# Optimization experiments

Hardware: AMD Instinct MI355X
Metric: run time of the kernel (lower is better)

## Reference

```python
import jax, jax.numpy as jnp
import numpy as np

B, CIN, COUT, H, W = 4, 256, 128, 64, 64

def conv1x1(x, w, b):
    # x: [B,C,H,W], w: [O,C], b: [O]
    return jnp.einsum('bchw,oc->bohw', x, w) + b[None, :, None, None]

def setup_inputs() -> dict:
    key = jax.random.key(0)
    ks = jax.random.split(key, 9)
    s_in = 1.0 / np.sqrt(CIN)
    s_out = 1.0 / np.sqrt(COUT)
    return {
        'x': jax.random.normal(ks[0], (B, CIN, H, W), dtype=jnp.float32),
        'w_theta': jax.random.normal(ks[1], (COUT, CIN), dtype=jnp.float32) * s_in,
        'b_theta': jax.random.normal(ks[2], (COUT,), dtype=jnp.float32) * s_in,
        'w_phi': jax.random.normal(ks[3], (COUT, CIN), dtype=jnp.float32) * s_in,
        'b_phi': jax.random.normal(ks[4], (COUT,), dtype=jnp.float32) * s_in,
        'w_g': jax.random.normal(ks[5], (COUT, CIN), dtype=jnp.float32) * s_in,
        'b_g': jax.random.normal(ks[6], (COUT,), dtype=jnp.float32) * s_in,
        'w_W': jax.random.normal(ks[7], (CIN, COUT), dtype=jnp.float32) * s_out,
        'b_W': jax.random.normal(ks[8], (CIN,), dtype=jnp.float32) * s_out,
    }

def reference(x, w_theta, b_theta, w_phi, b_phi, w_g, b_g, w_W, b_W):
    b, c, h, w = x.shape
    n = h * w
    co = w_theta.shape[0]
    theta_x = conv1x1(x, w_theta, b_theta).reshape(b, co, n).transpose(0, 2, 1)  # [B,N,Co]
    phi_x = conv1x1(x, w_phi, b_phi).reshape(b, co, n)                            # [B,Co,N]
    g_x = conv1x1(x, w_g, b_g).reshape(b, co, n).transpose(0, 2, 1)               # [B,N,Co]
    scores = jnp.einsum('bnc,bcm->bnm', theta_x, phi_x)                           # [B,N,N]
    attn = jax.nn.softmax(scores, axis=-1)
    y = jnp.einsum('bnm,bmc->bnc', attn, g_x)                                     # [B,N,Co]
    y = y.transpose(0, 2, 1).reshape(b, co, h, w)
    z = conv1x1(y, w_W, b_W) + x
    return z
```

## Files before the change

### kernel.cpp

```cpp
#include <hip/hip_runtime.h>

#define B_    4
#define C_    256
#define O_    128
#define N_    4096
#define THW   256
#define TILES 64

typedef __attribute__((ext_vector_type(8))) _Float16 f16x8;
typedef __attribute__((ext_vector_type(4))) float    f32x4;

struct __align__(8) us4 { unsigned short x, y, z, w; };

__device__ __forceinline__ float bf2f(unsigned short u) {
    unsigned v = ((unsigned)u) << 16;
    union { unsigned u; float f; } c; c.u = v; return c.f;
}
__device__ __forceinline__ unsigned short f2bf(float f) {
    union { float f; unsigned u; } c; c.f = f;
    unsigned r = c.u + 0x7fffu + ((c.u >> 16) & 1u);
    return (unsigned short)(r >> 16);
}
__device__ __forceinline__ unsigned short f2h(float f) {
    _Float16 h = (_Float16)f;
    union { _Float16 h; unsigned short s; } c; c.h = h; return c.s;
}
__device__ __forceinline__ float h2f(unsigned short s) {
    union { unsigned short s; _Float16 h; } c; c.s = s; return (float)c.h;
}

__device__ __forceinline__ void load4f(const void* base, size_t idx, int isf32, float o[4]) {
    if (isf32) {
        float4 v = *(const float4*)((const float*)base + idx);
        o[0] = v.x; o[1] = v.y; o[2] = v.z; o[3] = v.w;
    } else {
        us4 v = *(const us4*)((const unsigned short*)base + idx);
        o[0] = bf2f(v.x); o[1] = bf2f(v.y); o[2] = bf2f(v.z); o[3] = bf2f(v.w);
    }
}
__device__ __forceinline__ float load1f(const void* base, size_t idx, int isf32) {
    return isf32 ? ((const float*)base)[idx] : bf2f(((const unsigned short*)base)[idx]);
}

__global__ __launch_bounds__(256) void detect_kernel(
    const unsigned short* __restrict__ xu, int* __restrict__ flag)
{
    __shared__ int cnt;
    if (threadIdx.x == 0) cnt = 0;
    __syncthreads();
    int local = 0;
    for (int i = threadIdx.x; i < 4096; i += 256) {
        unsigned short u = xu[2 * i];
        int e = (u >> 7) & 0xFF;
        if (e == 0xFF || e >= 0x90 || (e > 0 && e <= 0x60)) local++;
    }
    atomicAdd(&cnt, local);
    __syncthreads();
    if (threadIdx.x == 0) *flag = (cnt > 1024) ? 1 : 0;
}

__global__ __launch_bounds__(256) void qkv_kernel(
    const void* __restrict__ x,
    const void* __restrict__ wt, const void* __restrict__ wp,
    const void* __restrict__ wg,
    const void* __restrict__ bt, const void* __restrict__ bp,
    const void* __restrict__ bg,
    const int*  __restrict__ flag,
    unsigned short* __restrict__ thph,
    unsigned short* __restrict__ gT)
{
    const int isf32 = *flag;
    const int jsel = blockIdx.y;
    const void* w  = jsel == 0 ? wt : (jsel == 1 ? wp : wg);
    const void* bi = jsel == 0 ? bt : (jsel == 1 ? bp : bg);
    const int b  = blockIdx.z;
    const int n0 = blockIdx.x * 64;
    const int tid  = threadIdx.x;
    const int wv   = tid >> 6, lane = tid & 63;
    const int quad = lane >> 4, l16 = lane & 15;

    __shared__ alignas(16) unsigned short smem[64 * 72 + 128 * 72];
    unsigned short (*As)[72] = (unsigned short(*)[72])smem;
    unsigned short (*Bs)[72] = (unsigned short(*)[72])(smem + 64 * 72);

    f32x4 acc[8];
    for (int i = 0; i < 8; i++) acc[i] = (f32x4)0.f;

    for (int kc = 0; kc < C_; kc += 64) {
        __syncthreads();
        for (int it = 0; it < 4; it++) {
            int l = it * 256 + tid;
            int c = l >> 4;
            int ng = l & 15;
            float v[4];
            load4f(x, (size_t)(b * C_ + kc + c) * N_ + n0 + ng * 4, isf32, v);
            int g = c >> 3, cl = c & 7;
            int swz = ((g ^ (ng & 7)) << 3) + cl;
            As[ng * 4 + 0][swz] = f2h(v[0]);
            As[ng * 4 + 1][swz] = f2h(v[1]);
            As[ng * 4 + 2][swz] = f2h(v[2]);
            As[ng * 4 + 3][swz] = f2h(v[3]);
        }
        for (int it = 0; it < 8; it++) {
            int l = it * 256 + tid;
            int j = l >> 4;
            int cg = l & 15;
            float v[4];
            load4f(w, (size_t)j * C_ + kc + cg * 4, isf32, v);
            Bs[j][cg * 4 + 0] = f2h(v[0]);
            Bs[j][cg * 4 + 1] = f2h(v[1]);
            Bs[j][cg * 4 + 2] = f2h(v[2]);
            Bs[j][cg * 4 + 3] = f2h(v[3]);
        }
        __syncthreads();
        for (int s = 0; s < 2; s++) {
            int row = wv * 16 + l16;
            int g2 = ((s * 4 + quad) ^ ((row >> 2) & 7)) << 3;
            f16x8 a = *(const f16x8*)&As[row][g2];
            for (int jt = 0; jt < 8; jt++) {
                f16x8 bb = *(const f16x8*)&Bs[jt * 16 + l16][s * 32 + quad * 8];
                acc[jt] = __builtin_amdgcn_mfma_f32_16x16x32_f16(a, bb, acc[jt], 0, 0, 0);
            }
        }
    }

    if (jsel < 2) {
        for (int jt = 0; jt < 8; jt++) {
            int j = jt * 16 + l16;
            float bias = load1f(bi, j, isf32);
            for (int r = 0; r < 4; r++) {
                int n = n0 + wv * 16 + quad * 4 + r;
                thph[(size_t)(b * N_ + n) * THW + jsel * O_ + j] = f2h(acc[jt][r] + bias);
            }
        }
    } else {
        unsigned short (*T)[68] = (unsigned short(*)[68])smem;
        __syncthreads();
        for (int jt = 0; jt < 8; jt++) {
            int j = jt * 16 + l16;
            float bias = load1f(bi, j, isf32);
            for (int r = 0; r < 4; r++) {
                int nl = wv * 16 + quad * 4 + r;
                T[j][nl] = f2h(acc[jt][r] + bias);
            }
        }
        __syncthreads();
        for (int it = 0; it < 8; it++) {
            int l = it * 256 + tid;
            int j = l >> 4;
            int ng = l & 15;
            *(us4*)(gT + ((size_t)(b * O_ + j)) * N_ + n0 + ng * 4) = *(const us4*)&T[j][ng * 4];
        }
    }
}

__global__ __launch_bounds__(512, 4) void attn_partial(
    const unsigned short* __restrict__ thph,
    const unsigned short* __restrict__ gT,
    unsigned short* __restrict__ partO,
    float* __restrict__ pm,
    float* __restrict__ pl,
    int S)
{
    const int b    = blockIdx.z;
    const int s_id = blockIdx.y;
    const int n0   = blockIdx.x * 128;
    const int tid  = threadIdx.x;
    const int wv   = tid >> 6, lane = tid & 63;
    const int quad = lane >> 4, l16 = lane & 15;

    const int t0 = (TILES * s_id) / S;
    const int t1 = (TILES * (s_id + 1)) / S;

    __shared__ alignas(16) unsigned short Ks[64][136];
    __shared__ alignas(16) unsigned short Gs[128][72];
    __shared__ alignas(16) unsigned short Ps[8][16][72];

    f16x8 qf[4];
    {
        int qrow = n0 + wv * 16 + l16;
        const unsigned short* qp = thph + (size_t)(b * N_ + qrow) * THW;
        for (int s = 0; s < 4; s++)
            qf[s] = *(const f16x8*)(qp + s * 32 + quad * 8);
    }

    f32x4 oacc[8];
    for (int i = 0; i < 8; i++) oacc[i] = (f32x4)0.f;
    float mstate = -INFINITY, lstate = 0.f;

    us4 kreg[4], greg[4];
    auto prefetch = [&](int mt) {
        int m0 = mt * 64;
        #pragma unroll
        for (int it = 0; it < 4; it++) {
            int l = it * 512 + tid;
            int mm = l >> 5, og = l & 31;
            kreg[it] = *(const us4*)(thph + (size_t)(b * N_ + m0 + mm) * THW + O_ + og * 4);
        }
        #pragma unroll
        for (int it = 0; it < 4; it++) {
            int l = it * 512 + tid;
            int o = l >> 4, ng = l & 15;
            greg[it] = *(const us4*)(gT + ((size_t)(b * O_ + o)) * N_ + m0 + ng * 4);
        }
    };
    prefetch(t0);

    for (int mt = t0; mt < t1; mt++) {
        __syncthreads();
        #pragma unroll
        for (int it = 0; it < 4; it++) {
            int l = it * 512 + tid;
            int mm = l >> 5, og = l & 31;
            *(us4*)&Ks[mm][og * 4] = kreg[it];
        }
        #pragma unroll
        for (int it = 0; it < 4; it++) {
            int l = it * 512 + tid;
            int o = l >> 4, ng = l & 15;
            *(us4*)&Gs[o][ng * 4] = greg[it];
        }
        __syncthreads();
        if (mt + 1 < t1) prefetch(mt + 1);

        f32x4 sacc[4];
        for (int kt = 0; kt < 4; kt++) sacc[kt] = (f32x4)0.f;
        for (int s = 0; s < 4; s++) {
            for (int kt = 0; kt < 4; kt++) {
                f16x8 kb = *(const f16x8*)&Ks[kt * 16 + l16][s * 32 + quad * 8];
                sacc[kt] = __builtin_amdgcn_mfma_f32_16x16x32_f16(kb, qf[s], sacc[kt], 0, 0, 0);
            }
        }

        float rm = fmaxf(fmaxf(fmaxf(sacc[0][0], sacc[0][1]), fmaxf(sacc[0][2], sacc[0][3])),
                         fmaxf(fmaxf(sacc[1][0], sacc[1][1]), fmaxf(sacc[1][2], sacc[1][3])));
        rm = fmaxf(rm, fmaxf(fmaxf(fmaxf(sacc[2][0], sacc[2][1]), fmaxf(sacc[2][2], sacc[2][3])),
                             fmaxf(fmaxf(sacc[3][0], sacc[3][1]), fmaxf(sacc[3][2], sacc[3][3]))));
        rm = fmaxf(rm, __shfl_xor(rm, 16));
        rm = fmaxf(rm, __shfl_xor(rm, 32));

        float mnew  = fmaxf(mstate, rm);
        float alpha = __expf(mstate - mnew);
        mstate = mnew;

        float rs = 0.f;
        #pragma unroll
        for (int kt = 0; kt < 4; kt++) {
            float p0 = __expf(sacc[kt][0] - mnew);
            float p1 = __expf(sacc[kt][1] - mnew);
            float p2 = __expf(sacc[kt][2] - mnew);
            float p3 = __expf(sacc[kt][3] - mnew);
            rs += (p0 + p1) + (p2 + p3);
            us4 pk;
            pk.x = f2h(p0); pk.y = f2h(p1); pk.z = f2h(p2); pk.w = f2h(p3);
            *(us4*)&Ps[wv][l16][kt * 16 + quad * 4] = pk;
        }
        rs += __shfl_xor(rs, 16);
        rs += __shfl_xor(rs, 32);
        lstate = lstate * alpha + rs;

        float av[4];
        #pragma unroll
        for (int r = 0; r < 4; r++) av[r] = __shfl(alpha, quad * 4 + r);
        #pragma unroll
        for (int jt = 0; jt < 8; jt++)
            #pragma unroll
            for (int r = 0; r < 4; r++) oacc[jt][r] *= av[r];

        for (int s = 0; s < 2; s++) {
            f16x8 pa = *(const f16x8*)&Ps[wv][l16][s * 32 + quad * 8];
            for (int jt = 0; jt < 8; jt++) {
                f16x8 gb = *(const f16x8*)&Gs[jt * 16 + l16][s * 32 + quad * 8];
                oacc[jt] = __builtin_amdgcn_mfma_f32_16x16x32_f16(pa, gb, oacc[jt], 0, 0, 0);
            }
        }
    }

    for (int r = 0; r < 4; r++) {
        int n = n0 + wv * 16 + quad * 4 + r;
        size_t rowb = ((size_t)(s_id * B_ + b) * N_ + n) * O_;
        for (int jt = 0; jt < 8; jt++)
            partO[rowb + jt * 16 + l16] = f2h(oacc[jt][r]);
    }
    if (quad == 0) {
        int n = n0 + wv * 16 + l16;
        pm[(size_t)(s_id * B_ + b) * N_ + n] = mstate;
        pl[(size_t)(s_id * B_ + b) * N_ + n] = lstate;
    }
}

__global__ __launch_bounds__(256) void merge_kernel(
    const unsigned short* __restrict__ partO,
    const float* __restrict__ pm, const float* __restrict__ pl,
    unsigned short* __restrict__ y,
    int S)
{
    int idx = blockIdx.x * 256 + threadIdx.x;
    int bn  = idx >> 5;
    int og  = idx & 31;
    const int BN = B_ * N_;

    float M = -INFINITY;
    for (int s = 0; s < S; s++) M = fmaxf(M, pm[(size_t)s * BN + bn]);
    float w[4];
    float L = 0.f;
    for (int s = 0; s < S; s++) {
        w[s] = __expf(pm[(size_t)s * BN + bn] - M);
        L += w[s] * pl[(size_t)s * BN + bn];
    }
    float inv = 1.0f / L;

    float a0 = 0.f, a1 = 0.f, a2 = 0.f, a3 = 0.f;
    for (int s = 0; s < S; s++) {
        us4 v = *(const us4*)(partO + ((size_t)s * BN + bn) * O_ + og * 4);
        a0 += h2f(v.x) * w[s];
        a1 += h2f(v.y) * w[s];
        a2 += h2f(v.z) * w[s];
        a3 += h2f(v.w) * w[s];
    }
    us4 r;
    r.x = f2h(a0 * inv); r.y = f2h(a1 * inv);
    r.z = f2h(a2 * inv); r.w = f2h(a3 * inv);
    *(us4*)(y + (size_t)bn * O_ + og * 4) = r;
}

__global__ __launch_bounds__(256) void out_kernel(
    const unsigned short* __restrict__ y,
    const void* __restrict__ wW,
    const void* __restrict__ bW,
    const void* __restrict__ x,
    const int*  __restrict__ flag,
    void* __restrict__ z)
{
    const int isf32 = *flag;
    const int b  = blockIdx.z;
    const int c0 = blockIdx.y * 64;
    const int n0 = blockIdx.x * 128;
    const int tid  = threadIdx.x;
    const int wv   = tid >> 6, lane = tid & 63;
    const int quad = lane >> 4, l16 = lane & 15;

    __shared__ alignas(16) unsigned short Ys[128][136];
    __shared__ alignas(16) unsigned short Ws[64][136];

    for (int it = 0; it < 16; it++) {
        int l = it * 256 + tid;
        int nn = l >> 5;
        int og = l & 31;
        us4 v = *(const us4*)(y + (size_t)(b * N_ + n0 + nn) * O_ + og * 4);
        *(us4*)&Ys[nn][og * 4] = v;
    }
    for (int it = 0; it < 8; it++) {
        int l = it * 256 + tid;
        int cc = l >> 5;
        int og = l & 31;
        float v[4];
        load4f(wW, (size_t)(c0 + cc) * O_ + og * 4, isf32, v);
        Ws[cc][og * 4 + 0] = f2h(v[0]);
        Ws[cc][og * 4 + 1] = f2h(v[1]);
        Ws[cc][og * 4 + 2] = f2h(v[2]);
        Ws[cc][og * 4 + 3] = f2h(v[3]);
    }
    __syncthreads();

    f32x4 acc[8];
    for (int i = 0; i < 8; i++) acc[i] = (f32x4)0.f;
    for (int s = 0; s < 4; s++) {
        f16x8 a = *(const f16x8*)&Ws[wv * 16 + l16][s * 32 + quad * 8];
        for (int nt = 0; nt < 8; nt++) {
            f16x8 bb = *(const f16x8*)&Ys[nt * 16 + l16][s * 32 + quad * 8];
            acc[nt] = __builtin_amdgcn_mfma_f32_16x16x32_f16(a, bb, acc[nt], 0, 0, 0);
        }
    }
    for (int r = 0; r < 4; r++) {
        int c = c0 + wv * 16 + quad * 4 + r;
        float bias = load1f(bW, c, isf32);
        for (int nt = 0; nt < 8; nt++) {
            int n = n0 + nt * 16 + l16;
            size_t idx = (size_t)(b * C_ + c) * N_ + n;
            float zv = acc[nt][r] + bias + load1f(x, idx, isf32);
            if (isf32) ((float*)z)[idx] = zv;
            else       ((unsigned short*)z)[idx] = f2bf(zv);
        }
    }
}

extern "C" void kernel_launch(void* const* d_in, const int* in_sizes, int n_in,
                              void* d_out, int out_size, void* d_ws, size_t ws_size,
                              hipStream_t stream) {
    const void* x  = d_in[0];
    const void* wt = d_in[1];
    const void* bt = d_in[2];
    const void* wp = d_in[3];
    const void* bp = d_in[4];
    const void* wg = d_in[5];
    const void* bg = d_in[6];
    const void* wW = d_in[7];
    const void* bW = d_in[8];

    const size_t base = 64 + 8388608  + 4194304 ;
    const size_t per_split = 4194304  + 131072 ;
    int S = 4;
    while (S > 1 && base + (size_t)S * per_split > ws_size) S--;

    char* p = (char*)d_ws;
    int* flag = (int*)p;                    p += 64;
    unsigned short* thph = (unsigned short*)p;  p += 8388608;
    unsigned short* gT   = (unsigned short*)p;  p += 4194304;
    unsigned short* partO = (unsigned short*)p; p += (size_t)S * 4194304;
    float* pm = (float*)p;                  p += (size_t)S * 65536;
    float* pl = (float*)p;
    unsigned short* y = gT;

    detect_kernel<<<1, 256, 0, stream>>>((const unsigned short*)x, flag);

    dim3 g1(N_ / 64, 3, B_);
    qkv_kernel<<<g1, 256, 0, stream>>>(x, wt, wp, wg, bt, bp, bg, flag, thph, gT);

    dim3 g2(N_ / 128, S, B_);
    attn_partial<<<g2, 512, 0, stream>>>(thph, gT, partO, pm, pl, S);

    merge_kernel<<<(B_ * N_ * 32) / 256, 256, 0, stream>>>(partO, pm, pl, y, S);

    dim3 g3(N_ / 128, C_ / 64, B_);
    out_kernel<<<g3, 256, 0, stream>>>(y, wW, bW, x, flag, d_out);
}
```

Baseline: 187.2 us.

## Fuse QKV projections into one block per tile and raise attention split count

The QKV projection kernel now computes theta, phi and g together in one 512-thread block per 64-pixel tile. The x tile is held in registers for the whole channel range, and the weight tile is double-buffered through registers and LDS. This removes the three-fold re-read and conversion of x and overlaps weight loads with MFMA work, at the cost of higher register pressure and scalar strided x loads. Separately, the key split count for attention rises from 4 to 6 (workspace permitting) to add parallelism, with more partial-output traffic in the merge.

```diff
diff --git a/kernel.cpp b/kernel.cpp
--- a/kernel.cpp
+++ b/kernel.cpp
@@ -59,7 +59,7 @@
     if (threadIdx.x == 0) *flag = (cnt > 1024) ? 1 : 0;
 }
 
-__global__ __launch_bounds__(256) void qkv_kernel(
+__global__ __launch_bounds__(512, 2) void qkv_kernel(
     const void* __restrict__ x,
     const void* __restrict__ wt, const void* __restrict__ wp,
     const void* __restrict__ wg,
@@ -70,87 +70,123 @@
     unsigned short* __restrict__ gT)
 {
     const int isf32 = *flag;
-    const int jsel = blockIdx.y;
-    const void* w  = jsel == 0 ? wt : (jsel == 1 ? wp : wg);
-    const void* bi = jsel == 0 ? bt : (jsel == 1 ? bp : bg);
-    const int b  = blockIdx.z;
+    const int b  = blockIdx.y;
     const int n0 = blockIdx.x * 64;
     const int tid  = threadIdx.x;
     const int wv   = tid >> 6, lane = tid & 63;
     const int quad = lane >> 4, l16 = lane & 15;
-
-    __shared__ alignas(16) unsigned short smem[64 * 72 + 128 * 72];
-    unsigned short (*As)[72] = (unsigned short(*)[72])smem;
-    unsigned short (*Bs)[72] = (unsigned short(*)[72])(smem + 64 * 72);
-
-    f32x4 acc[8];
-    for (int i = 0; i < 8; i++) acc[i] = (f32x4)0.f;
-
-    for (int kc = 0; kc < C_; kc += 64) {
+    const int wv_n = wv & 1;
+    const int wv_jg = wv >> 1;
+
+    __shared__ alignas(16) unsigned short smem[2 * 384 * 40];
+    unsigned short (*Bs)[384][40] = (unsigned short(*)[384][40])smem;
+    unsigned short (*T)[68] = (unsigned short(*)[68])smem;
+
+    f16x8 areg[2][8];
+    #pragma unroll
+    for (int a = 0; a < 2; a++) {
+        int n = n0 + (wv_n * 2 + a) * 16 + l16;
+        #pragma unroll
+        for (int s8 = 0; s8 < 8; s8++) {
+            f16x8 fr;
+            #pragma unroll
+            for (int e = 0; e < 8; e++) {
+                int c = s8 * 32 + quad * 8 + e;
+                fr[e] = (_Float16)load1f(x, (size_t)(b * C_ + c) * N_ + n, isf32);
+            }
+            areg[a][s8] = fr;
+        }
+    }
+
+    us4 wreg[2][6];
+    auto loadW = [&](int s8, int slot) {
+        #pragma unroll
+        for (int it = 0; it < 6; it++) {
+            int idx = it * 512 + tid;
+            int j = idx >> 3, cg = idx & 7;
+            const void* wsel = j < 128 ? wt : (j < 256 ? wp : wg);
+            float v[4];
+            load4f(wsel, (size_t)(j & 127) * C_ + s8 * 32 + cg * 4, isf32, v);
+            us4 h;
+            h.x = f2h(v[0]); h.y = f2h(v[1]); h.z = f2h(v[2]); h.w = f2h(v[3]);
+            wreg[slot][it] = h;
+        }
+    };
+    auto stageW = [&](int buf, int slot) {
+        #pragma unroll
+        for (int it = 0; it < 6; it++) {
+            int idx = it * 512 + tid;
+            int j = idx >> 3, cg = idx & 7;
+            *(us4*)&Bs[buf][0][j * 40 + cg * 4] = wreg[slot][it];
+        }
+    };
+
+    loadW(0, 0);
+    loadW(1, 1);
+    stageW(0, 0);
+
+    f32x4 acc[2][6];
+    #pragma unroll
+    for (int a = 0; a < 2; a++)
+        for (int jt = 0; jt < 6; jt++) acc[a][jt] = (f32x4)0.f;
+
+    for (int i = 0; i < 8; i++) {
         __syncthreads();
-        for (int it = 0; it < 4; it++) {
-            int l = it * 256 + tid;
-            int c = l >> 4;
-            int ng = l & 15;
-            float v[4];
-            load4f(x, (size_t)(b * C_ + kc + c) * N_ + n0 + ng * 4, isf32, v);
-            int g = c >> 3, cl = c & 7;
-            int swz = ((g ^ (ng & 7)) << 3) + cl;
-            As[ng * 4 + 0][swz] = f2h(v[0]);
-            As[ng * 4 + 1][swz] = f2h(v[1]);
-            As[ng * 4 + 2][swz] = f2h(v[2]);
-            As[ng * 4 + 3][swz] = f2h(v[3]);
-        }
-        for (int it = 0; it < 8; it++) {
-            int l = it * 256 + tid;
-            int j = l >> 4;
-            int cg = l & 15;
-            float v[4];
-            load4f(w, (size_t)j * C_ + kc + cg * 4, isf32, v);
-            Bs[j][cg * 4 + 0] = f2h(v[0]);
-            Bs[j][cg * 4 + 1] = f2h(v[1]);
-            Bs[j][cg * 4 + 2] = f2h(v[2]);
-            Bs[j][cg * 4 + 3] = f2h(v[3]);
-        }
-        __syncthreads();
-        for (int s = 0; s < 2; s++) {
-            int row = wv * 16 + l16;
-            int g2 = ((s * 4 + quad) ^ ((row >> 2) & 7)) << 3;
-            f16x8 a = *(const f16x8*)&As[row][g2];
-            for (int jt = 0; jt < 8; jt++) {
-                f16x8 bb = *(const f16x8*)&Bs[jt * 16 + l16][s * 32 + quad * 8];
-                acc[jt] = __builtin_amdgcn_mfma_f32_16x16x32_f16(a, bb, acc[jt], 0, 0, 0);
+        int buf = i & 1;
+        f16x8 bfrag[6];
+        #pragma unroll
+        for (int jt = 0; jt < 6; jt++)
+            bfrag[jt] = *(const f16x8*)&Bs[buf][0][(wv_jg * 96 + jt * 16 + l16) * 40 + quad * 8];
+        #pragma unroll
+        for (int a = 0; a < 2; a++)
+            #pragma unroll
+            for (int jt = 0; jt < 6; jt++)
+                acc[a][jt] = __builtin_amdgcn_mfma_f32_16x16x32_f16(
+                    areg[a][i], bfrag[jt], acc[a][jt], 0, 0, 0);
+        if (i + 1 < 8) {
+            stageW((i + 1) & 1, (i + 1) & 1);
+            if (i + 2 < 8) loadW(i + 2, i & 1);
+        }
+    }
+
+    #pragma unroll
+    for (int a = 0; a < 2; a++) {
+        #pragma unroll
+        for (int jt = 0; jt < 6; jt++) {
+            int j = wv_jg * 96 + jt * 16 + l16;
+            if (j < 256) {
+                const void* bsel = j < 128 ? bt : bp;
+                float bias = load1f(bsel, j & 127, isf32);
+                #pragma unroll
+                for (int r = 0; r < 4; r++) {
+                    int n = n0 + (wv_n * 2 + a) * 16 + quad * 4 + r;
+                    thph[(size_t)(b * N_ + n) * THW + j] = f2h(acc[a][jt][r] + bias);
+                }
             }
         }
     }
-
-    if (jsel < 2) {
-        for (int jt = 0; jt < 8; jt++) {
-            int j = jt * 16 + l16;
-            float bias = load1f(bi, j, isf32);
-            for (int r = 0; r < 4; r++) {
-                int n = n0 + wv * 16 + quad * 4 + r;
-                thph[(size_t)(b * N_ + n) * THW + jsel * O_ + j] = f2h(acc[jt][r] + bias);
+    __syncthreads();
+    #pragma unroll
+    for (int a = 0; a < 2; a++) {
+        #pragma unroll
+        for (int jt = 0; jt < 6; jt++) {
+            int j = wv_jg * 96 + jt * 16 + l16;
+            if (j >= 256) {
+                float bias = load1f(bg, j - 256, isf32);
+                #pragma unroll
+                for (int r = 0; r < 4; r++) {
+                    int nl = (wv_n * 2 + a) * 16 + quad * 4 + r;
+                    T[j - 256][nl] = f2h(acc[a][jt][r] + bias);
+                }
             }
         }
-    } else {
-        unsigned short (*T)[68] = (unsigned short(*)[68])smem;
-        __syncthreads();
-        for (int jt = 0; jt < 8; jt++) {
-            int j = jt * 16 + l16;
-            float bias = load1f(bi, j, isf32);
-            for (int r = 0; r < 4; r++) {
-                int nl = wv * 16 + quad * 4 + r;
-                T[j][nl] = f2h(acc[jt][r] + bias);
-            }
-        }
-        __syncthreads();
-        for (int it = 0; it < 8; it++) {
-            int l = it * 256 + tid;
-            int j = l >> 4;
-            int ng = l & 15;
-            *(us4*)(gT + ((size_t)(b * O_ + j)) * N_ + n0 + ng * 4) = *(const us4*)&T[j][ng * 4];
-        }
+    }
+    __syncthreads();
+    #pragma unroll
+    for (int it = 0; it < 4; it++) {
+        int idx = it * 512 + tid;
+        int j = idx >> 4, ng = idx & 15;
+        *(us4*)(gT + ((size_t)(b * O_ + j)) * N_ + n0 + ng * 4) = *(const us4*)&T[j][ng * 4];
     }
 }
 
@@ -302,7 +338,7 @@
 
     float M = -INFINITY;
     for (int s = 0; s < S; s++) M = fmaxf(M, pm[(size_t)s * BN + bn]);
-    float w[4];
+    float w[8];
     float L = 0.f;
     for (int s = 0; s < S; s++) {
         w[s] = __expf(pm[(size_t)s * BN + bn] - M);
@@ -400,7 +436,7 @@
 
     const size_t base = 64 + 8388608  + 4194304 ;
     const size_t per_split = 4194304  + 131072 ;
-    int S = 4;
+    int S = 6;
     while (S > 1 && base + (size_t)S * per_split > ws_size) S--;
 
     char* p = (char*)d_ws;
@@ -414,8 +450,8 @@
 
     detect_kernel<<<1, 256, 0, stream>>>((const unsigned short*)x, flag);
 
-    dim3 g1(N_ / 64, 3, B_);
-    qkv_kernel<<<g1, 256, 0, stream>>>(x, wt, wp, wg, bt, bp, bg, flag, thph, gT);
+    dim3 g1(N_ / 64, B_);
+    qkv_kernel<<<g1, 512, 0, stream>>>(x, wt, wp, wg, bt, bp, bg, flag, thph, gT);
 
     dim3 g2(N_ / 128, S, B_);
     attn_partial<<<g2, 512, 0, stream>>>(thph, gT, partO, pm, pl, S);
```

New measurement: 237.9 us. 1.27x slower.
